# Kernel optimization log

Measured on AMD Instinct MI355X. Metric: run time of the kernel, lower is better.

The kernel has to match this reference:

```python
import jax, jax.numpy as jnp
import numpy as np

N_EXPERTS = 64
TOP_K = 8
ALPHA = 0.01
EMBED_DIM = 2048


def setup_inputs() -> dict:
    key = jax.random.key(0)
    k1, k2 = jax.random.split(key)
    hidden_states = jax.random.normal(k1, (4, 8192, EMBED_DIM), dtype=jnp.float32)
    # router weight, torch init-style scale
    weight = jax.random.normal(k2, (N_EXPERTS, EMBED_DIM), dtype=jnp.float32) / np.sqrt(EMBED_DIM)
    return {"hidden_states": hidden_states, "weight": weight}


def reference(hidden_states, weight):
    # flatten tokens: [B,S,D] -> [N,D]
    x = hidden_states.reshape(-1, hidden_states.shape[-1])
    # router logits: [N,E]
    logits = jnp.einsum('nd,ed->ne', x, weight)
    scores = jax.nn.softmax(logits, axis=-1)
    # top-k routing weights and expert ids (torch uses sorted=False; order is immaterial)
    topk_weight, topk_idx = jax.lax.top_k(scores, TOP_K)
    # aux load-balance loss (training path, alpha > 0)
    counts = jnp.bincount(topk_idx.reshape(-1), length=N_EXPERTS).astype(scores.dtype)
    ce = counts / topk_idx.size  # fraction of assignments per expert
    Pi = scores.mean(axis=0)     # mean router prob per expert
    aux_loss = jnp.sum(Pi * ce * N_EXPERTS) * ALPHA
    return topk_idx, topk_weight, aux_loss
```

## Files before the change

### kernel.cpp

```cpp
#include <hip/hip_runtime.h>

#define EMBED_D 2048
#define N_EXP   64
#define K_TOP   8
#define TOK_BLK 64
#define THREADS 512
#define NCHUNK  32
#define CHUNK_B 24576

typedef __attribute__((ext_vector_type(8))) short bf16x8;
typedef __attribute__((ext_vector_type(4))) float f32x4;

__device__ __forceinline__ uint bf16_rne(float x) {
    uint u = __float_as_uint(x);
    return (u + 0x7fffu + ((u >> 16) & 1u)) >> 16;
}
__device__ __forceinline__ float bf16f(uint h) { return __uint_as_float(h << 16); }

__device__ __forceinline__ void stage16(const void* g, void* l)
{
    typedef __attribute__((address_space(1))) const unsigned int gu32;
    typedef __attribute__((address_space(3))) unsigned int lu32;
    __builtin_amdgcn_global_load_lds((gu32*)g, (lu32*)l, 16, 0, 0);
}

__global__ void w_prep(const float* __restrict__ W, ushort* __restrict__ WF)
{
    const int e = blockIdx.x;
    const int t = threadIdx.x;
    const float4 a = *(const float4*)(W + (size_t)e * EMBED_D + t * 8);
    const float4 b = *(const float4*)(W + (size_t)e * EMBED_D + t * 8 + 4);
    const float ev[8] = {a.x, a.y, a.z, a.w, b.x, b.y, b.z, b.w};
    ushort h[8], m[8], l[8];
#pragma unroll
    for (int j = 0; j < 8; ++j) {
        const uint hh = bf16_rne(ev[j]);
        const float r1 = ev[j] - bf16f(hh);
        const uint mm = bf16_rne(r1);
        const uint ll = bf16_rne(r1 - bf16f(mm));
        h[j] = (ushort)hh; m[j] = (ushort)mm; l[j] = (ushort)ll;
    }
    const int c  = t >> 3;
    const int kk = (t >> 2) & 1;
    const int g  = t & 3;
    const int lane = g * 16 + (e & 15);
    const int n    = e >> 4;
    const size_t base = (size_t)c * 12288 + (size_t)kk * 2048 + (size_t)n * 512 + (size_t)lane * 8;
    ushort4* H = (ushort4*)(WF + base);
    ushort4* M = (ushort4*)(WF + base + 4096);
    ushort4* L = (ushort4*)(WF + base + 8192);
    H[0] = make_ushort4(h[0], h[1], h[2], h[3]); H[1] = make_ushort4(h[4], h[5], h[6], h[7]);
    M[0] = make_ushort4(m[0], m[1], m[2], m[3]); M[1] = make_ushort4(m[4], m[5], m[6], m[7]);
    L[0] = make_ushort4(l[0], l[1], l[2], l[3]); L[1] = make_ushort4(l[4], l[5], l[6], l[7]);
}

__global__ __launch_bounds__(THREADS, 4) void moe_gate_main(
    const float*  __restrict__ X,
    const ushort* __restrict__ WF,
    float* __restrict__ out,
    float* __restrict__ ws,
    int n_tok)
{
    __shared__ __align__(16) char smem[2 * CHUNK_B];
    __shared__ float sInvZ[TOK_BLK];
    __shared__ float sCnt[N_EXP];
    __shared__ float sColp[8][N_EXP];

    const int tid  = threadIdx.x;
    const int lane = tid & 63;
    const int wv   = __builtin_amdgcn_readfirstlane(tid >> 6);
    const int tg   = wv & 3;
    const int eh   = wv >> 2;
    const int row  = lane & 15;
    const int g    = lane >> 4;
    const int t0   = blockIdx.x * TOK_BLK;
    const int tok  = t0 + tg * 16 + row;

    const float* xp = X + (size_t)tok * EMBED_D + g * 8;
    const char*  wf = (const char*)WF;

    f32x4 acc[2];
    acc[0] = (f32x4){0.f, 0.f, 0.f, 0.f};
    acc[1] = (f32x4){0.f, 0.f, 0.f, 0.f};

    float4 xq[4];
#pragma unroll
    for (int i = 0; i < 2; ++i) {
        xq[2 * i]     = *(const float4*)(xp + i * 32);
        xq[2 * i + 1] = *(const float4*)(xp + i * 32 + 4);
    }

    {
        const char* gs = wf + (size_t)wv * 3072 + lane * 16;
        char* ld = smem + wv * 3072;
#pragma unroll
        for (int i = 0; i < 3; ++i)
            stage16(gs + i * 1024, ld + i * 1024);
    }
    __syncthreads();

    for (int c = 0; c < NCHUNK; ++c) {
        const int cur = c & 1;

        if (c + 1 < NCHUNK) {
            const char* gs = wf + (size_t)(c + 1) * CHUNK_B + wv * 3072 + lane * 16;
            char* ld = smem + (cur ^ 1) * CHUNK_B + wv * 3072;
#pragma unroll
            for (int i = 0; i < 3; ++i)
                stage16(gs + i * 1024, ld + i * 1024);
        }

        bf16x8 ah[2], am[2], al[2];
#pragma unroll
        for (int kk = 0; kk < 2; ++kk) {
            const float ev[8] = {xq[2*kk].x, xq[2*kk].y, xq[2*kk].z, xq[2*kk].w,
                                 xq[2*kk+1].x, xq[2*kk+1].y, xq[2*kk+1].z, xq[2*kk+1].w};
#pragma unroll
            for (int j = 0; j < 8; ++j) {
                const uint h  = bf16_rne(ev[j]);
                const float r1 = ev[j] - bf16f(h);
                const uint m  = bf16_rne(r1);
                const uint l  = bf16_rne(r1 - bf16f(m));
                ah[kk][j] = (short)h; am[kk][j] = (short)m; al[kk][j] = (short)l;
            }
        }

        if (c + 1 < NCHUNK) {
#pragma unroll
            for (int i = 0; i < 2; ++i) {
                xq[2 * i]     = *(const float4*)(xp + (c + 1) * 64 + i * 32);
                xq[2 * i + 1] = *(const float4*)(xp + (c + 1) * 64 + i * 32 + 4);
            }
        }

        const char* wb = smem + cur * CHUNK_B;
#pragma unroll
        for (int kk = 0; kk < 2; ++kk) {
#pragma unroll
            for (int nl = 0; nl < 2; ++nl) {
                const int n = eh * 2 + nl;
                const char* bp = wb + (size_t)(kk * 4 + n) * 1024 + lane * 16;
                const bf16x8 bh = *(const bf16x8*)(bp);
                const bf16x8 bm = *(const bf16x8*)(bp + 8192);
                const bf16x8 bl = *(const bf16x8*)(bp + 16384);
                acc[nl] = __builtin_amdgcn_mfma_f32_16x16x32_bf16(ah[kk], bh, acc[nl], 0, 0, 0);
                acc[nl] = __builtin_amdgcn_mfma_f32_16x16x32_bf16(am[kk], bh, acc[nl], 0, 0, 0);
                acc[nl] = __builtin_amdgcn_mfma_f32_16x16x32_bf16(ah[kk], bm, acc[nl], 0, 0, 0);
                acc[nl] = __builtin_amdgcn_mfma_f32_16x16x32_bf16(al[kk], bh, acc[nl], 0, 0, 0);
                acc[nl] = __builtin_amdgcn_mfma_f32_16x16x32_bf16(ah[kk], bl, acc[nl], 0, 0, 0);
                acc[nl] = __builtin_amdgcn_mfma_f32_16x16x32_bf16(am[kk], bm, acc[nl], 0, 0, 0);
            }
        }
        __syncthreads();
    }

    float (*Lp)[N_EXP + 1] = (float (*)[N_EXP + 1])smem;
#pragma unroll
    for (int nl = 0; nl < 2; ++nl)
#pragma unroll
        for (int r = 0; r < 4; ++r)
            Lp[tg * 16 + g * 4 + r][(eh * 2 + nl) * 16 + row] = acc[nl][r];
    if (tid < N_EXP) sCnt[tid] = 0.f;
    __syncthreads();

    if (tid < TOK_BLK) {
        const int t = tid;
        float mx = -1e30f;
        for (int e = 0; e < N_EXP; ++e)
            mx = fmaxf(mx, Lp[t][e]);
        float Z = 0.f;
        float tv[K_TOP]; int ti[K_TOP];
#pragma unroll
        for (int j = 0; j < K_TOP; ++j) { tv[j] = -1e30f; ti[j] = 0; }
        for (int e = 0; e < N_EXP; ++e) {
            const float s = __expf(Lp[t][e] - mx);
            Lp[t][e] = s;
            Z += s;
            float v = s; int id = e;
#pragma unroll
            for (int j = 0; j < K_TOP; ++j) {
                if (v > tv[j]) {
                    float fv = tv[j]; tv[j] = v; v = fv;
                    int   fi = ti[j]; ti[j] = id; id = fi;
                }
            }
        }
        const float invZ = 1.0f / Z;
        sInvZ[t] = invZ;
        const size_t ob = (size_t)(t0 + t) * K_TOP;
        const size_t wo = (size_t)n_tok * K_TOP;
#pragma unroll
        for (int j = 0; j < K_TOP; ++j) {
            out[ob + j]      = (float)ti[j];
            out[wo + ob + j] = tv[j] * invZ;
            atomicAdd(&sCnt[ti[j]], 1.0f);
        }
    }
    __syncthreads();

    {
        const int e = tid & 63, g2 = tid >> 6;
        float s = 0.f;
#pragma unroll
        for (int i = 0; i < 8; ++i) {
            const int t = g2 * 8 + i;
            s += Lp[t][e] * sInvZ[t];
        }
        sColp[g2][e] = s;
    }
    __syncthreads();
    if (tid < N_EXP) {
        float s = 0.f;
#pragma unroll
        for (int g2 = 0; g2 < 8; ++g2) s += sColp[g2][tid];
        atomicAdd(&ws[64 + tid], s);
        atomicAdd(&ws[tid], sCnt[tid]);
    }
}

__global__ void moe_aux(const float* __restrict__ ws, float* __restrict__ out, int n_tok)
{
    const int e = threadIdx.x;
    const float counts = ws[e];
    const float ssum   = ws[64 + e];
    const float Pi = ssum / (float)n_tok;
    const float ce = counts / ((float)n_tok * (float)K_TOP);
    float term = Pi * ce * (float)N_EXP;
    for (int off = 32; off; off >>= 1) term += __shfl_down(term, off);
    if (e == 0) out[(size_t)2 * n_tok * K_TOP] = term * 0.01f;
}

extern "C" void kernel_launch(void* const* d_in, const int* in_sizes, int n_in,
                              void* d_out, int out_size, void* d_ws, size_t ws_size,
                              hipStream_t stream)
{
    const float* X = (const float*)d_in[0];
    const float* W = (const float*)d_in[1];
    float* out = (float*)d_out;
    float* ws  = (float*)d_ws;
    const int n_tok = in_sizes[0] / EMBED_D;

    ushort* WF = (ushort*)(ws + 256);

    hipMemsetAsync(ws, 0, 2 * N_EXP * sizeof(float), stream);
    w_prep<<<N_EXP, 256, 0, stream>>>(W, WF);
    moe_gate_main<<<n_tok / TOK_BLK, THREADS, 0, stream>>>(X, WF, out, ws, n_tok);
    moe_aux<<<1, 64, 0, stream>>>(ws, out, n_tok);
}
```

Baseline: 407.8 us.

## Stage X tiles through LDS with swizzle and give each wave two token tiles

X is now loaded asynchronously into LDS with global_load_lds, in an XOR-swizzled layout, alongside the weight chunk. Previously each thread read X with direct register loads. Blocks drop to 256 threads (4 waves) and each wave computes two 16-token tiles, so each weight fragment read from LDS is reused across two MFMA A operands. The K chunk is halved to 32 and the W prep layout is changed to match. The split into three bf16 parts uses perm-based packing, and the last part is truncated rather than rounded. The aim is to cut global load latency on the critical path and LDS traffic per MFMA, at the cost of fewer waves per block and more chunk iterations and barriers.

```diff
diff --git a/kernel.cpp b/kernel.cpp
--- a/kernel.cpp
+++ b/kernel.cpp
@@ -1,12 +1,14 @@
 #include <hip/hip_runtime.h>
 
-#define EMBED_D 2048
-#define N_EXP   64
-#define K_TOP   8
-#define TOK_BLK 64
-#define THREADS 512
-#define NCHUNK  32
-#define CHUNK_B 24576
+#define EMBED_D  2048
+#define N_EXP    64
+#define K_TOP    8
+#define TOK_BLK  64
+#define THREADS  256
+#define NCHUNK   64
+#define WCHUNK_B 12288
+#define XCHUNK_B 8192
+#define BUF_B    (WCHUNK_B + XCHUNK_B)
 
 typedef __attribute__((ext_vector_type(8))) short bf16x8;
 typedef __attribute__((ext_vector_type(4))) float f32x4;
@@ -22,6 +24,28 @@
     typedef __attribute__((address_space(1))) const unsigned int gu32;
     typedef __attribute__((address_space(3))) unsigned int lu32;
     __builtin_amdgcn_global_load_lds((gu32*)g, (lu32*)l, 16, 0, 0);
+}
+
+__device__ __forceinline__ void split3(float4 u, float4 v, bf16x8& H, bf16x8& M, bf16x8& L)
+{
+    const float x[8] = {u.x, u.y, u.z, u.w, v.x, v.y, v.z, v.w};
+    uint hw[8], mw[8], lw[8];
+#pragma unroll
+    for (int j = 0; j < 8; ++j) {
+        const uint ux = __float_as_uint(x[j]);
+        hw[j] = (ux + 0x7fffu + ((ux >> 16) & 1u)) & 0xffff0000u;
+        const float r1 = x[j] - __uint_as_float(hw[j]);
+        const uint ur = __float_as_uint(r1);
+        mw[j] = (ur + 0x7fffu + ((ur >> 16) & 1u)) & 0xffff0000u;
+        lw[j] = __float_as_uint(r1 - __uint_as_float(mw[j]));
+    }
+    uint* hp = (uint*)&H; uint* mp = (uint*)&M; uint* lp = (uint*)&L;
+#pragma unroll
+    for (int w = 0; w < 4; ++w) {
+        hp[w] = __builtin_amdgcn_perm(hw[2 * w + 1], hw[2 * w], 0x07060302u);
+        mp[w] = __builtin_amdgcn_perm(mw[2 * w + 1], mw[2 * w], 0x07060302u);
+        lp[w] = __builtin_amdgcn_perm(lw[2 * w + 1], lw[2 * w], 0x07060302u);
+    }
 }
 
 __global__ void w_prep(const float* __restrict__ W, ushort* __restrict__ WF)
@@ -40,15 +64,14 @@
         const uint ll = bf16_rne(r1 - bf16f(mm));
         h[j] = (ushort)hh; m[j] = (ushort)mm; l[j] = (ushort)ll;
     }
-    const int c  = t >> 3;
-    const int kk = (t >> 2) & 1;
-    const int g  = t & 3;
+    const int c = t >> 2;
+    const int g = t & 3;
     const int lane = g * 16 + (e & 15);
     const int n    = e >> 4;
-    const size_t base = (size_t)c * 12288 + (size_t)kk * 2048 + (size_t)n * 512 + (size_t)lane * 8;
+    const size_t base = (size_t)c * 6144 + (size_t)n * 512 + (size_t)lane * 8;
     ushort4* H = (ushort4*)(WF + base);
-    ushort4* M = (ushort4*)(WF + base + 4096);
-    ushort4* L = (ushort4*)(WF + base + 8192);
+    ushort4* M = (ushort4*)(WF + base + 2048);
+    ushort4* L = (ushort4*)(WF + base + 4096);
     H[0] = make_ushort4(h[0], h[1], h[2], h[3]); H[1] = make_ushort4(h[4], h[5], h[6], h[7]);
     M[0] = make_ushort4(m[0], m[1], m[2], m[3]); M[1] = make_ushort4(m[4], m[5], m[6], m[7]);
     L[0] = make_ushort4(l[0], l[1], l[2], l[3]); L[1] = make_ushort4(l[4], l[5], l[6], l[7]);
@@ -61,41 +84,52 @@
     float* __restrict__ ws,
     int n_tok)
 {
-    __shared__ __align__(16) char smem[2 * CHUNK_B];
+    __shared__ __align__(16) char smem[2 * BUF_B];
     __shared__ float sInvZ[TOK_BLK];
     __shared__ float sCnt[N_EXP];
-    __shared__ float sColp[8][N_EXP];
+    __shared__ float sColp[4][N_EXP];
 
     const int tid  = threadIdx.x;
     const int lane = tid & 63;
     const int wv   = __builtin_amdgcn_readfirstlane(tid >> 6);
-    const int tg   = wv & 3;
-    const int eh   = wv >> 2;
+    const int tg   = wv & 1;
+    const int eh   = wv >> 1;
     const int row  = lane & 15;
     const int g    = lane >> 4;
     const int t0   = blockIdx.x * TOK_BLK;
-    const int tok  = t0 + tg * 16 + row;
-
-    const float* xp = X + (size_t)tok * EMBED_D + g * 8;
-    const char*  wf = (const char*)WF;
-
-    f32x4 acc[2];
-    acc[0] = (f32x4){0.f, 0.f, 0.f, 0.f};
-    acc[1] = (f32x4){0.f, 0.f, 0.f, 0.f};
-
-    float4 xq[4];
-#pragma unroll
-    for (int i = 0; i < 2; ++i) {
-        xq[2 * i]     = *(const float4*)(xp + i * 32);
-        xq[2 * i + 1] = *(const float4*)(xp + i * 32 + 4);
-    }
-
+
+    const char* wsrc = (const char*)WF + (size_t)wv * 1024 + lane * 16;
+    const float* xsrc0; const float* xsrc1;
     {
-        const char* gs = wf + (size_t)wv * 3072 + lane * 16;
-        char* ld = smem + wv * 3072;
-#pragma unroll
-        for (int i = 0; i < 3; ++i)
-            stage16(gs + i * 1024, ld + i * 1024);
+        const int q0 = wv * 64 + lane,       t0k = q0 >> 3;
+        const int q1 = 256 + wv * 64 + lane, t1k = q1 >> 3;
+        xsrc0 = X + (size_t)(t0 + t0k) * EMBED_D + ((q0 & 7) ^ (t0k & 7)) * 4;
+        xsrc1 = X + (size_t)(t0 + t1k) * EMBED_D + ((q1 & 7) ^ (t1k & 7)) * 4;
+    }
+
+    int xo[2][2];
+#pragma unroll
+    for (int ai = 0; ai < 2; ++ai) {
+        const int tk = tg * 32 + ai * 16 + row;
+        const int s  = tk & 7;
+        xo[ai][0] = tk * 128 + ((2 * g)     ^ s) * 16;
+        xo[ai][1] = tk * 128 + ((2 * g + 1) ^ s) * 16;
+    }
+
+    f32x4 acc[2][2];
+#pragma unroll
+    for (int ai = 0; ai < 2; ++ai)
+#pragma unroll
+        for (int nl = 0; nl < 2; ++nl)
+            acc[ai][nl] = (f32x4){0.f, 0.f, 0.f, 0.f};
+
+    {
+        char* bb = smem;
+#pragma unroll
+        for (int r = 0; r < 3; ++r)
+            stage16(wsrc + r * 4096, bb + r * 4096 + wv * 1024);
+        stage16(xsrc0, bb + WCHUNK_B + wv * 1024);
+        stage16(xsrc1, bb + WCHUNK_B + 4096 + wv * 1024);
     }
     __syncthreads();
 
@@ -103,63 +137,54 @@
         const int cur = c & 1;
 
         if (c + 1 < NCHUNK) {
-            const char* gs = wf + (size_t)(c + 1) * CHUNK_B + wv * 3072 + lane * 16;
-            char* ld = smem + (cur ^ 1) * CHUNK_B + wv * 3072;
-#pragma unroll
-            for (int i = 0; i < 3; ++i)
-                stage16(gs + i * 1024, ld + i * 1024);
-        }
+            char* bb = smem + (cur ^ 1) * BUF_B;
+            const char* wsc = wsrc + (size_t)(c + 1) * WCHUNK_B;
+#pragma unroll
+            for (int r = 0; r < 3; ++r)
+                stage16(wsc + r * 4096, bb + r * 4096 + wv * 1024);
+            stage16(xsrc0 + (c + 1) * 32, bb + WCHUNK_B + wv * 1024);
+            stage16(xsrc1 + (c + 1) * 32, bb + WCHUNK_B + 4096 + wv * 1024);
+        }
+
+        const char* bb = smem + cur * BUF_B;
+        const char* xb = bb + WCHUNK_B;
 
         bf16x8 ah[2], am[2], al[2];
 #pragma unroll
-        for (int kk = 0; kk < 2; ++kk) {
-            const float ev[8] = {xq[2*kk].x, xq[2*kk].y, xq[2*kk].z, xq[2*kk].w,
-                                 xq[2*kk+1].x, xq[2*kk+1].y, xq[2*kk+1].z, xq[2*kk+1].w};
-#pragma unroll
-            for (int j = 0; j < 8; ++j) {
-                const uint h  = bf16_rne(ev[j]);
-                const float r1 = ev[j] - bf16f(h);
-                const uint m  = bf16_rne(r1);
-                const uint l  = bf16_rne(r1 - bf16f(m));
-                ah[kk][j] = (short)h; am[kk][j] = (short)m; al[kk][j] = (short)l;
+        for (int ai = 0; ai < 2; ++ai) {
+            const float4 u = *(const float4*)(xb + xo[ai][0]);
+            const float4 v = *(const float4*)(xb + xo[ai][1]);
+            split3(u, v, ah[ai], am[ai], al[ai]);
+        }
+
+#pragma unroll
+        for (int nl = 0; nl < 2; ++nl) {
+            const int n = eh * 2 + nl;
+            const char* bp = bb + (size_t)n * 1024 + lane * 16;
+            const bf16x8 bh = *(const bf16x8*)(bp);
+            const bf16x8 bm = *(const bf16x8*)(bp + 4096);
+            const bf16x8 bl = *(const bf16x8*)(bp + 8192);
+#pragma unroll
+            for (int ai = 0; ai < 2; ++ai) {
+                acc[ai][nl] = __builtin_amdgcn_mfma_f32_16x16x32_bf16(ah[ai], bh, acc[ai][nl], 0, 0, 0);
+                acc[ai][nl] = __builtin_amdgcn_mfma_f32_16x16x32_bf16(am[ai], bh, acc[ai][nl], 0, 0, 0);
+                acc[ai][nl] = __builtin_amdgcn_mfma_f32_16x16x32_bf16(ah[ai], bm, acc[ai][nl], 0, 0, 0);
+                acc[ai][nl] = __builtin_amdgcn_mfma_f32_16x16x32_bf16(al[ai], bh, acc[ai][nl], 0, 0, 0);
+                acc[ai][nl] = __builtin_amdgcn_mfma_f32_16x16x32_bf16(ah[ai], bl, acc[ai][nl], 0, 0, 0);
+                acc[ai][nl] = __builtin_amdgcn_mfma_f32_16x16x32_bf16(am[ai], bm, acc[ai][nl], 0, 0, 0);
             }
         }
-
-        if (c + 1 < NCHUNK) {
-#pragma unroll
-            for (int i = 0; i < 2; ++i) {
-                xq[2 * i]     = *(const float4*)(xp + (c + 1) * 64 + i * 32);
-                xq[2 * i + 1] = *(const float4*)(xp + (c + 1) * 64 + i * 32 + 4);
-            }
-        }
-
-        const char* wb = smem + cur * CHUNK_B;
-#pragma unroll
-        for (int kk = 0; kk < 2; ++kk) {
-#pragma unroll
-            for (int nl = 0; nl < 2; ++nl) {
-                const int n = eh * 2 + nl;
-                const char* bp = wb + (size_t)(kk * 4 + n) * 1024 + lane * 16;
-                const bf16x8 bh = *(const bf16x8*)(bp);
-                const bf16x8 bm = *(const bf16x8*)(bp + 8192);
-                const bf16x8 bl = *(const bf16x8*)(bp + 16384);
-                acc[nl] = __builtin_amdgcn_mfma_f32_16x16x32_bf16(ah[kk], bh, acc[nl], 0, 0, 0);
-                acc[nl] = __builtin_amdgcn_mfma_f32_16x16x32_bf16(am[kk], bh, acc[nl], 0, 0, 0);
-                acc[nl] = __builtin_amdgcn_mfma_f32_16x16x32_bf16(ah[kk], bm, acc[nl], 0, 0, 0);
-                acc[nl] = __builtin_amdgcn_mfma_f32_16x16x32_bf16(al[kk], bh, acc[nl], 0, 0, 0);
-                acc[nl] = __builtin_amdgcn_mfma_f32_16x16x32_bf16(ah[kk], bl, acc[nl], 0, 0, 0);
-                acc[nl] = __builtin_amdgcn_mfma_f32_16x16x32_bf16(am[kk], bm, acc[nl], 0, 0, 0);
-            }
-        }
         __syncthreads();
     }
 
     float (*Lp)[N_EXP + 1] = (float (*)[N_EXP + 1])smem;
 #pragma unroll
-    for (int nl = 0; nl < 2; ++nl)
-#pragma unroll
-        for (int r = 0; r < 4; ++r)
-            Lp[tg * 16 + g * 4 + r][(eh * 2 + nl) * 16 + row] = acc[nl][r];
+    for (int ai = 0; ai < 2; ++ai)
+#pragma unroll
+        for (int nl = 0; nl < 2; ++nl)
+#pragma unroll
+            for (int r = 0; r < 4; ++r)
+                Lp[tg * 32 + ai * 16 + g * 4 + r][(eh * 2 + nl) * 16 + row] = acc[ai][nl][r];
     if (tid < N_EXP) sCnt[tid] = 0.f;
     __syncthreads();
 
@@ -202,8 +227,8 @@
         const int e = tid & 63, g2 = tid >> 6;
         float s = 0.f;
 #pragma unroll
-        for (int i = 0; i < 8; ++i) {
-            const int t = g2 * 8 + i;
+        for (int i = 0; i < 16; ++i) {
+            const int t = g2 * 16 + i;
             s += Lp[t][e] * sInvZ[t];
         }
         sColp[g2][e] = s;
@@ -212,7 +237,7 @@
     if (tid < N_EXP) {
         float s = 0.f;
 #pragma unroll
-        for (int g2 = 0; g2 < 8; ++g2) s += sColp[g2][tid];
+        for (int g2 = 0; g2 < 4; ++g2) s += sColp[g2][tid];
         atomicAdd(&ws[64 + tid], s);
         atomicAdd(&ws[tid], sCnt[tid]);
     }
```

Measured after the change: 419.3 us. +2.8%, slower.
